# Optimization experiments

Hardware: AMD Instinct MI355X
Metric: run time of the kernel (lower is better)

The kernel has to match this reference:

```python
import jax, jax.numpy as jnp
import numpy as np
import math

B, L, D = 8, 2048, 256


def setup_inputs() -> dict:
    key = jax.random.key(0)
    ks = jax.random.split(key, 8)
    return {
        "query": jax.random.normal(ks[0], (B, L, D), dtype=jnp.float32),
        "key": jax.random.normal(ks[1], (B, L, D), dtype=jnp.float32),
        "value": jax.random.normal(ks[2], (B, L, D), dtype=jnp.float32),
        "mask": jax.random.randint(ks[3], (B, L), 0, 2, dtype=jnp.int32),
        "Wq_w": jax.random.normal(ks[4], (D, D), dtype=jnp.float32) * 0.05,
        "Wq_b": jax.random.normal(ks[5], (D,), dtype=jnp.float32) * 0.05,
        "Wk_w": jax.random.normal(ks[6], (D, D), dtype=jnp.float32) * 0.05,
        "Wk_b": jax.random.normal(ks[7], (D,), dtype=jnp.float32) * 0.05,
    }


def reference(query, key, value, mask, Wq_w, Wq_b, Wk_w, Wk_b):
    d = query.shape[-1]
    q = query @ Wq_w.T + Wq_b            # [B, Lq, D]
    k = key @ Wk_w.T + Wk_b              # [B, Lk, D]
    scores = jnp.einsum("bqd,bkd->bqk", q, k) / math.sqrt(d)  # [B, Lq, Lk]
    m = mask.astype(scores.dtype)[:, None, :]                  # [B, 1, Lk]
    # multiplicative then additive masking, as in original
    scores = jnp.where(m == 0, jnp.asarray(-1e9, scores.dtype), scores * m)
    attn = jax.nn.softmax(scores, axis=-1)
    return jnp.einsum("bqk,bkd->bqd", attn, value)
```

## Files before the change

kernel.cpp:

```cpp
#include <hip/hip_runtime.h>
#include <stdint.h>
#include <stddef.h>

#define B_ 8
#define L_ 2048
#define D_ 256
#define KRANGE 512
#define KTILE 32
#define NITER 16

typedef __bf16 bf16x8 __attribute__((ext_vector_type(8)));
typedef float floatx4 __attribute__((ext_vector_type(4)));
typedef float floatx16 __attribute__((ext_vector_type(16)));
typedef _Float16 half4_t __attribute__((ext_vector_type(4)));
typedef _Float16 half8_t __attribute__((ext_vector_type(8)));

__device__ __forceinline__ short f2bf(float f) {
    union { float f; uint32_t u; } v; v.f = f;
    return (short)((v.u + 0x8000u) >> 16);
}

__device__ __forceinline__ uint32_t pack2bf(float a, float b) {
    union { float f; uint32_t u; } x, y; x.f = a; y.f = b;
    return ((x.u + 0x8000u) >> 16) | ((y.u + 0x8000u) & 0xFFFF0000u);
}

__device__ __forceinline__ uint32_t cvtpk_bf16(float lo, float hi2) {
    uint32_t w;
    asm("v_cvt_pk_bf16_f32 %0, %1, %2" : "=v"(w) : "v"(lo), "v"(hi2));
    return w;
}

__device__ __forceinline__ void pl32swap(uint32_t &a, uint32_t &b) {
    asm("v_permlane32_swap_b32 %0, %1" : "+v"(a), "+v"(b));
}

__device__ __forceinline__ void async16(const void* g, void* l) {
    __builtin_amdgcn_global_load_lds(
        (__attribute__((address_space(1))) void*)g,
        (__attribute__((address_space(3))) void*)l,
        16, 0, 0);
}

__global__ __launch_bounds__(256, 3) void proj_kernel(
    const float* __restrict__ Xq, const float* __restrict__ Xk,
    const float* __restrict__ Wq, const float* __restrict__ Wk,
    const float* __restrict__ bq, const float* __restrict__ bk,
    short* __restrict__ Oq, short* __restrict__ Ok)
{
    const float* X    = blockIdx.y ? Xk : Xq;
    const float* W    = blockIdx.y ? Wk : Wq;
    const float* bias = blockIdx.y ? bk : bq;
    short* Out        = blockIdx.y ? Ok : Oq;

    __shared__ uint32_t As[2][64 * 20];
    __shared__ uint32_t Ws[2][256 * 20];

    const int tid  = threadIdx.x;
    const int wid  = tid >> 6;
    const int lane = tid & 63;
    const int m16  = lane & 15;
    const int quad = lane >> 4;
    const int row0 = blockIdx.x * 64;
    const int ar = tid >> 2, cg = tid & 3;

    floatx4 acc[16];
    const floatx4 z4 = {0.f, 0.f, 0.f, 0.f};
#pragma unroll
    for (int i = 0; i < 16; i++) acc[i] = z4;

    {
        const float* srcA = X + (size_t)(row0 + ar) * D_ + cg * 8;
        float4 a = *(const float4*)srcA, b2 = *(const float4*)(srcA + 4);
        uint4 u; u.x = pack2bf(a.x, a.y); u.y = pack2bf(a.z, a.w);
        u.z = pack2bf(b2.x, b2.y); u.w = pack2bf(b2.z, b2.w);
        *(uint4*)&As[0][ar * 20 + cg * 4] = u;
#pragma unroll
        for (int p = 0; p < 4; p++) {
            const float* srcW = W + (size_t)(p * 64 + ar) * D_ + cg * 8;
            float4 wa = *(const float4*)srcW, wb = *(const float4*)(srcW + 4);
            uint4 w; w.x = pack2bf(wa.x, wa.y); w.y = pack2bf(wa.z, wa.w);
            w.z = pack2bf(wb.x, wb.y); w.w = pack2bf(wb.z, wb.w);
            *(uint4*)&Ws[0][(p * 64 + ar) * 20 + cg * 4] = w;
        }
    }
    __syncthreads();

    for (int kc = 0; kc < 8; kc++) {
        const int buf = kc & 1;
        float4 na, nb, nwa[4], nwb[4];
        if (kc < 7) {
            const int k1 = (kc + 1) * 32;
            const float* srcA = X + (size_t)(row0 + ar) * D_ + k1 + cg * 8;
            na = *(const float4*)srcA; nb = *(const float4*)(srcA + 4);
#pragma unroll
            for (int p = 0; p < 4; p++) {
                const float* srcW = W + (size_t)(p * 64 + ar) * D_ + k1 + cg * 8;
                nwa[p] = *(const float4*)srcW; nwb[p] = *(const float4*)(srcW + 4);
            }
        }
        bf16x8 af = *(const bf16x8*)&As[buf][(wid * 16 + m16) * 20 + quad * 4];
#pragma unroll
        for (int n = 0; n < 16; n++) {
            bf16x8 bfr = *(const bf16x8*)&Ws[buf][(n * 16 + m16) * 20 + quad * 4];
            acc[n] = __builtin_amdgcn_mfma_f32_16x16x32_bf16(af, bfr, acc[n], 0, 0, 0);
        }
        if (kc < 7) {
            uint4 u; u.x = pack2bf(na.x, na.y); u.y = pack2bf(na.z, na.w);
            u.z = pack2bf(nb.x, nb.y); u.w = pack2bf(nb.z, nb.w);
            *(uint4*)&As[buf ^ 1][ar * 20 + cg * 4] = u;
#pragma unroll
            for (int p = 0; p < 4; p++) {
                uint4 w; w.x = pack2bf(nwa[p].x, nwa[p].y); w.y = pack2bf(nwa[p].z, nwa[p].w);
                w.z = pack2bf(nwb[p].x, nwb[p].y); w.w = pack2bf(nwb[p].z, nwb[p].w);
                *(uint4*)&Ws[buf ^ 1][(p * 64 + ar) * 20 + cg * 4] = w;
            }
        }
        __syncthreads();
    }
#pragma unroll
    for (int n = 0; n < 16; n++) {
        const int col = n * 16 + m16;
        const float bv = bias[col];
#pragma unroll
        for (int r = 0; r < 4; r++) {
            const int row = row0 + wid * 16 + quad * 4 + r;
            Out[(size_t)row * D_ + col] = f2bf(acc[n][r] + bv);
        }
    }
}

__global__ __launch_bounds__(256, 2) void vtrans_kernel(
    const float* __restrict__ V, short* __restrict__ Vt)
{
    __shared__ uint32_t T[256 * 20];
    const int tid = threadIdx.x;
    const int b  = blockIdx.y;
    const int l0 = blockIdx.x * 32;
    const int r2 = tid >> 4;
    const int dg = tid & 15;
    const int lp = r2 ^ ((dg & 3) << 2);
#pragma unroll
    for (int p = 0; p < 4; p++) {
        int d0 = (dg + p * 16) * 4;
        const float* src = V + ((size_t)b * L_ + l0 + r2 * 2) * D_ + d0;
        float4 e0 = *(const float4*)src;
        float4 e1 = *(const float4*)(src + D_);
        T[(d0 + 0) * 20 + lp] = pack2bf(e0.x, e1.x);
        T[(d0 + 1) * 20 + lp] = pack2bf(e0.y, e1.y);
        T[(d0 + 2) * 20 + lp] = pack2bf(e0.z, e1.z);
        T[(d0 + 3) * 20 + lp] = pack2bf(e0.w, e1.w);
    }
    __syncthreads();
#pragma unroll
    for (int p = 0; p < 4; p++) {
        int d = (tid >> 2) + p * 64;
        int c = tid & 3;
        int cp = c ^ ((d >> 2) & 3);
        uint4 u = *(const uint4*)&T[d * 20 + cp * 4];
        *(uint4*)(Vt + ((size_t)b * D_ + d) * L_ + l0 + c * 8) = u;
    }
}

__global__ __launch_bounds__(512, 2) void flash_kernel(
    const short* __restrict__ Qb, const short* __restrict__ Kb,
    const short* __restrict__ Vt, const int* __restrict__ mask,
    float* __restrict__ Out, _Float16* __restrict__ Part,
    float* __restrict__ Lpart)
{
    __shared__ short Ks[3][KTILE * 256];
    __shared__ short Vs[3][256 * KTILE];

    const int tid  = threadIdx.x;
    const int wid  = tid >> 6;
    const int lane = tid & 63;
    const int l31  = lane & 31;
    const int hi   = lane >> 5;
    const int b  = blockIdx.x;
    const int yb = blockIdx.y;
    const int q0 = yb * 256;
    const int z  = blockIdx.z;

    const char* kgb = (const char*)(Kb + ((size_t)b * L_ + z * KRANGE) * D_);
    const char* vgb = (const char*)(Vt + (size_t)b * D_ * L_ + z * KRANGE);
    const int*  mg  = mask + b * L_ + z * KRANGE;

    bf16x8 qf[16];
    {
        const short* qrow = Qb + ((size_t)b * L_ + q0 + wid * 32 + l31) * D_ + hi * 8;
#pragma unroll
        for (int dt = 0; dt < 16; dt++)
            qf[dt] = *(const bf16x8*)(qrow + dt * 16);
    }

    uint32_t mbits = 0;
#pragma unroll
    for (int t = 0; t < NITER; t++)
        mbits |= (mg[t * KTILE + l31] != 0 ? 1u : 0u) << t;

    floatx16 o[8];
#pragma unroll
    for (int n = 0; n < 8; n++)
#pragma unroll
        for (int r = 0; r < 16; r++) o[n][r] = 0.f;
    float rsum = 0.f;

    const int KBb = l31 * 512 + ((((l31 & 7) ^ ((l31 >> 3) & 3)) ^ hi) << 4);
    const int VBb = l31 * 64 + (((((l31 >> 1) & 3) ^ ((l31 >> 3) & 1)) ^ hi) << 4);

    int koff[2], voff[2];
#pragma unroll
    for (int c = 0; c < 2; c++) {
        int row = wid * 4 + c * 2 + hi;
        int gk = l31 ^ (row & 7) ^ ((row >> 3) & 3);
        koff[c] = row * 512 + gk * 16;
        int d = (wid * 2 + c) * 16 + (lane >> 2);
        int gv = (lane & 3) ^ ((lane >> 3) & 3) ^ ((lane >> 5) & 1);
        voff[c] = d * (L_ * 2) + gv * 16;
    }

#pragma unroll
    for (int c = 0; c < 2; c++) {
        async16(kgb + koff[c], (char*)&Ks[0][0] + (wid * 2 + c) * 1024);
        async16(vgb + voff[c], (char*)&Vs[2][0] + (wid * 2 + c) * 1024);
        async16(kgb + (KTILE * D_ * 2) + koff[c], (char*)&Ks[1][0] + (wid * 2 + c) * 1024);
        async16(vgb + voff[c], (char*)&Vs[0][0] + (wid * 2 + c) * 1024);
    }
    __builtin_amdgcn_s_waitcnt(0x0F70);
    __syncthreads();

    const float C2 = 0.09016844f;
    bf16x8 pfA, pfB;
    {
        union { uint32_t u[4]; bf16x8 v; } zz;
        zz.u[0] = 0; zz.u[1] = 0; zz.u[2] = 0; zz.u[3] = 0;
        pfA = zz.v; pfB = zz.v;
    }

    short* kCur = &Ks[0][0]; short* kNxt = &Ks[1][0]; short* kDst = &Ks[2][0];
    short* vP   = &Vs[2][0]; short* vQ   = &Vs[0][0]; short* vR   = &Vs[1][0];

    for (int t = 0; t < NITER; t++) {
        {
            const char* kp = kgb + (size_t)((t + 2) & 15) * (KTILE * D_ * 2);
            const char* vp = vgb + (size_t)((t + 1) & 15) * (KTILE * 2);
#pragma unroll
            for (int c = 0; c < 2; c++) {
                async16(kp + koff[c], (char*)kDst + (wid * 2 + c) * 1024);
                async16(vp + voff[c], (char*)vR + (wid * 2 + c) * 1024);
            }
        }

        const char* kl = (const char*)kCur;
        floatx16 s0, s1;
#pragma unroll
        for (int r = 0; r < 16; r++) { s0[r] = 0.f; s1[r] = 0.f; }
        __builtin_amdgcn_s_setprio(1);
#pragma unroll
        for (int dt = 0; dt < 16; dt += 2) {
            bf16x8 kf0 = *(const bf16x8*)(kl + (KBb ^ (dt << 5)));
            bf16x8 kf1 = *(const bf16x8*)(kl + (KBb ^ ((dt + 1) << 5)));
            s0 = __builtin_amdgcn_mfma_f32_32x32x16_bf16(kf0, qf[dt], s0, 0, 0, 0);
            s1 = __builtin_amdgcn_mfma_f32_32x32x16_bf16(kf1, qf[dt + 1], s1, 0, 0, 0);
        }

        const char* vl = (const char*)vP;
#pragma unroll
        for (int n = 0; n < 8; n++) {
            bf16x8 vf0 = *(const bf16x8*)(vl + (VBb ^ (n << 11)));
            bf16x8 vf1 = *(const bf16x8*)(vl + (VBb ^ ((n << 11) | 32)));
            o[n] = __builtin_amdgcn_mfma_f32_32x32x16_bf16(pfA, vf0, o[n], 0, 0, 0);
            o[n] = __builtin_amdgcn_mfma_f32_32x32x16_bf16(pfB, vf1, o[n], 0, 0, 0);
        }
        __builtin_amdgcn_s_setprio(0);

        uint32_t mb = (uint32_t)__ballot((mbits >> t) & 1) >> (hi * 4);
        uint32_t w[8];
#pragma unroll
        for (int i = 0; i < 8; i++) {
            const int r0 = 2 * i, r1 = 2 * i + 1;
            const int k0 = (r0 & 3) + 8 * (r0 >> 2);
            float sv0 = s0[r0] + s1[r0];
            float sv1 = s0[r1] + s1[r1];
            float e0 = ((mb >> k0) & 1) ? exp2f(sv0 * C2) : 0.f;
            float e1 = ((mb >> (k0 + 1)) & 1) ? exp2f(sv1 * C2) : 0.f;
            rsum += e0 + e1;
            w[i] = cvtpk_bf16(e0, e1);
        }
        pl32swap(w[0], w[2]); pl32swap(w[1], w[3]);
        pl32swap(w[4], w[6]); pl32swap(w[5], w[7]);
        {
            union { uint32_t u[4]; bf16x8 v; } ua, ub;
            ua.u[0] = w[0]; ua.u[1] = w[1]; ua.u[2] = w[2]; ua.u[3] = w[3];
            ub.u[0] = w[4]; ub.u[1] = w[5]; ub.u[2] = w[6]; ub.u[3] = w[7];
            pfA = ua.v; pfB = ub.v;
        }

        asm volatile("s_waitcnt vmcnt(4)" ::: "memory");
        __builtin_amdgcn_s_barrier();
        asm volatile("" ::: "memory");

        short* tk = kCur; kCur = kNxt; kNxt = kDst; kDst = tk;
        short* tv = vP;   vP = vQ;     vQ = vR;     vR = tv;
    }

    {
        const char* vl = (const char*)vP;
        __builtin_amdgcn_s_setprio(1);
#pragma unroll
        for (int n = 0; n < 8; n++) {
            bf16x8 vf0 = *(const bf16x8*)(vl + (VBb ^ (n << 11)));
            bf16x8 vf1 = *(const bf16x8*)(vl + (VBb ^ ((n << 11) | 32)));
            o[n] = __builtin_amdgcn_mfma_f32_32x32x16_bf16(pfA, vf0, o[n], 0, 0, 0);
            o[n] = __builtin_amdgcn_mfma_f32_32x32x16_bf16(pfB, vf1, o[n], 0, 0, 0);
        }
        __builtin_amdgcn_s_setprio(0);
    }

    rsum += __shfl_xor(rsum, 32);

    const size_t BLD = (size_t)B_ * L_ * D_;
    const size_t rowbase = (size_t)b * L_ + q0 + wid * 32;
    if (z == 0) {
        float* po = Out + rowbase * D_;
#pragma unroll
        for (int n = 0; n < 8; n++)
#pragma unroll
            for (int r = 0; r < 16; r++) {
                int q = (r & 3) + 8 * (r >> 2) + 4 * hi;
                po[(size_t)q * D_ + n * 32 + l31] = o[n][r];
            }
    } else {
        _Float16* pp = Part + (size_t)(z - 1) * BLD;
#pragma unroll
        for (int n = 0; n < 8; n++)
#pragma unroll
            for (int h2 = 0; h2 < 2; h2++) {
                half8_t hv;
#pragma unroll
                for (int i = 0; i < 8; i++) hv[i] = (_Float16)o[n][h2 * 8 + i];
                size_t cidx = ((((size_t)((b * 8 + yb) * 8 + wid)) * 8 + n) * 2 + h2) * 64 + lane;
                *(half8_t*)(pp + cidx * 8) = hv;
            }
    }
    if (lane < 32) {
        Lpart[(size_t)z * (B_ * L_) + rowbase + lane] = rsum;
    }
}

__global__ __launch_bounds__(256) void norm_kernel(
    float* __restrict__ Out, const _Float16* __restrict__ Part,
    const float* __restrict__ Lpart)
{
    const int gid  = blockIdx.x * 256 + threadIdx.x;
    const int lane = gid & 63;
    const int h2   = (gid >> 6) & 1;
    const int n    = (gid >> 7) & 7;
    const int w    = (gid >> 10) & 7;
    const int yb   = (gid >> 13) & 7;
    const int b    = gid >> 16;
    const int l31  = lane & 31, hi = lane >> 5;
    const int d    = n * 32 + l31;
    const int rowbase = b * L_ + yb * 256 + w * 32;
    const size_t BLD = (size_t)B_ * L_ * D_;
    const int BL = B_ * L_;

    float acc[8];
#pragma unroll
    for (int i = 0; i < 8; i++) acc[i] = 0.f;
#pragma unroll
    for (int zz = 0; zz < 3; zz++) {
        half8_t hv = *(const half8_t*)(Part + zz * BLD + (size_t)gid * 8);
#pragma unroll
        for (int i = 0; i < 8; i++) acc[i] += (float)hv[i];
    }
#pragma unroll
    for (int i = 0; i < 8; i++) {
        const int r = h2 * 8 + i;
        const int q = (r & 3) + 8 * (r >> 2) + 4 * hi;
        const int row = rowbase + q;
        float l = Lpart[row] + Lpart[BL + row] + Lpart[2 * BL + row] + Lpart[3 * BL + row];
        const size_t off = (size_t)row * D_ + d;
        Out[off] = (Out[off] + acc[i]) / l;
    }
}

extern "C" void kernel_launch(void* const* d_in, const int* in_sizes, int n_in,
                              void* d_out, int out_size, void* d_ws, size_t ws_size,
                              hipStream_t stream) {
    const float* query = (const float*)d_in[0];
    const float* key   = (const float*)d_in[1];
    const float* value = (const float*)d_in[2];
    const int*   mask  = (const int*)d_in[3];
    const float* Wq_w  = (const float*)d_in[4];
    const float* Wq_b  = (const float*)d_in[5];
    const float* Wk_w  = (const float*)d_in[6];
    const float* Wk_b  = (const float*)d_in[7];
    float* out = (float*)d_out;

    const size_t BLD = (size_t)B_ * L_ * D_;
    short* qb = (short*)d_ws;
    short* kb = qb + BLD;
    short* vt = kb + BLD;
    _Float16* part = (_Float16*)(vt + BLD);
    float* lpart = (float*)(part + 3 * BLD);

    proj_kernel<<<dim3(256, 2), 256, 0, stream>>>(query, key, Wq_w, Wk_w, Wq_b, Wk_b, qb, kb);
    vtrans_kernel<<<dim3(64, 8), 256, 0, stream>>>(value, vt);
    flash_kernel<<<dim3(8, 8, 4), 512, 0, stream>>>(qb, kb, vt, mask, out, part, lpart);
    norm_kernel<<<dim3((B_ * L_ * D_ / 8) / 256), 256, 0, stream>>>(out, part, lpart);
}
```

Baseline: 167.8 us.

## Fuse projection, V transpose, flash attention and normalization into one cooperative kernel

Replaces four separate kernel launches with a single cooperative kernel of 256 blocks that runs the V transpose, the Q/K projection (retiled to 128 rows per block), flash attention and the split-K normalization as phases separated by grid-wide syncs. The aim is to remove launch overhead and inter-kernel gaps. In exchange it adds the cost of grid.sync, limits the projection and normalization phases to 256 blocks (fewer than before), and raises LDS use to a 96KB static buffer, which may constrain occupancy.

```diff
diff --git a/kernel.cpp b/kernel.cpp
--- a/kernel.cpp
+++ b/kernel.cpp
@@ -1,6 +1,9 @@
 #include <hip/hip_runtime.h>
+#include <hip/hip_cooperative_groups.h>
 #include <stdint.h>
 #include <stddef.h>
+
+namespace cg = cooperative_groups;
 
 #define B_ 8
 #define L_ 2048
@@ -12,7 +15,6 @@
 typedef __bf16 bf16x8 __attribute__((ext_vector_type(8)));
 typedef float floatx4 __attribute__((ext_vector_type(4)));
 typedef float floatx16 __attribute__((ext_vector_type(16)));
-typedef _Float16 half4_t __attribute__((ext_vector_type(4)));
 typedef _Float16 half8_t __attribute__((ext_vector_type(8)));
 
 __device__ __forceinline__ short f2bf(float f) {
@@ -42,346 +44,358 @@
         16, 0, 0);
 }
 
-__global__ __launch_bounds__(256, 3) void proj_kernel(
-    const float* __restrict__ Xq, const float* __restrict__ Xk,
-    const float* __restrict__ Wq, const float* __restrict__ Wk,
-    const float* __restrict__ bq, const float* __restrict__ bk,
-    short* __restrict__ Oq, short* __restrict__ Ok)
+extern "C" __global__ __launch_bounds__(512, 2) void fused_kernel(
+    const float* __restrict__ query, const float* __restrict__ key,
+    const float* __restrict__ value, const int* __restrict__ mask,
+    const float* __restrict__ Wq_w, const float* __restrict__ Wq_b,
+    const float* __restrict__ Wk_w, const float* __restrict__ Wk_b,
+    short* __restrict__ qb, short* __restrict__ kb, short* __restrict__ vt,
+    float* __restrict__ out, _Float16* __restrict__ part,
+    float* __restrict__ lpart)
 {
-    const float* X    = blockIdx.y ? Xk : Xq;
-    const float* W    = blockIdx.y ? Wk : Wq;
-    const float* bias = blockIdx.y ? bk : bq;
-    short* Out        = blockIdx.y ? Ok : Oq;
-
-    __shared__ uint32_t As[2][64 * 20];
-    __shared__ uint32_t Ws[2][256 * 20];
-
-    const int tid  = threadIdx.x;
-    const int wid  = tid >> 6;
-    const int lane = tid & 63;
-    const int m16  = lane & 15;
-    const int quad = lane >> 4;
-    const int row0 = blockIdx.x * 64;
-    const int ar = tid >> 2, cg = tid & 3;
-
-    floatx4 acc[16];
-    const floatx4 z4 = {0.f, 0.f, 0.f, 0.f};
-#pragma unroll
-    for (int i = 0; i < 16; i++) acc[i] = z4;
+    __shared__ char smem[98304];
+
+    cg::grid_group grid = cg::this_grid();
+
+    const int tid = threadIdx.x;
+    const int bid = blockIdx.x + blockIdx.y * 8 + blockIdx.z * 64;
 
     {
-        const float* srcA = X + (size_t)(row0 + ar) * D_ + cg * 8;
-        float4 a = *(const float4*)srcA, b2 = *(const float4*)(srcA + 4);
-        uint4 u; u.x = pack2bf(a.x, a.y); u.y = pack2bf(a.z, a.w);
-        u.z = pack2bf(b2.x, b2.y); u.w = pack2bf(b2.z, b2.w);
-        *(uint4*)&As[0][ar * 20 + cg * 4] = u;
+        uint32_t* T = (uint32_t*)smem + (tid >> 8) * (256 * 20);
+        const int t2 = tid & 255;
+        const int vb = bid * 2 + (tid >> 8);
+        const int b  = vb >> 6;
+        const int l0 = (vb & 63) * 32;
+        const int r2 = t2 >> 4;
+        const int dg = t2 & 15;
+        const int lp = r2 ^ ((dg & 3) << 2);
 #pragma unroll
         for (int p = 0; p < 4; p++) {
-            const float* srcW = W + (size_t)(p * 64 + ar) * D_ + cg * 8;
-            float4 wa = *(const float4*)srcW, wb = *(const float4*)(srcW + 4);
-            uint4 w; w.x = pack2bf(wa.x, wa.y); w.y = pack2bf(wa.z, wa.w);
-            w.z = pack2bf(wb.x, wb.y); w.w = pack2bf(wb.z, wb.w);
-            *(uint4*)&Ws[0][(p * 64 + ar) * 20 + cg * 4] = w;
+            int d0 = (dg + p * 16) * 4;
+            const float* src = value + ((size_t)b * L_ + l0 + r2 * 2) * D_ + d0;
+            float4 e0 = *(const float4*)src;
+            float4 e1 = *(const float4*)(src + D_);
+            T[(d0 + 0) * 20 + lp] = pack2bf(e0.x, e1.x);
+            T[(d0 + 1) * 20 + lp] = pack2bf(e0.y, e1.y);
+            T[(d0 + 2) * 20 + lp] = pack2bf(e0.z, e1.z);
+            T[(d0 + 3) * 20 + lp] = pack2bf(e0.w, e1.w);
+        }
+        __syncthreads();
+#pragma unroll
+        for (int p = 0; p < 4; p++) {
+            int d = (t2 >> 2) + p * 64;
+            int c = t2 & 3;
+            int cp = c ^ ((d >> 2) & 3);
+            uint4 u = *(const uint4*)&T[d * 20 + cp * 4];
+            *(uint4*)(vt + ((size_t)b * D_ + d) * L_ + l0 + c * 8) = u;
         }
     }
     __syncthreads();
 
-    for (int kc = 0; kc < 8; kc++) {
-        const int buf = kc & 1;
-        float4 na, nb, nwa[4], nwb[4];
-        if (kc < 7) {
-            const int k1 = (kc + 1) * 32;
-            const float* srcA = X + (size_t)(row0 + ar) * D_ + k1 + cg * 8;
-            na = *(const float4*)srcA; nb = *(const float4*)(srcA + 4);
-#pragma unroll
-            for (int p = 0; p < 4; p++) {
-                const float* srcW = W + (size_t)(p * 64 + ar) * D_ + k1 + cg * 8;
-                nwa[p] = *(const float4*)srcW; nwb[p] = *(const float4*)(srcW + 4);
-            }
-        }
-        bf16x8 af = *(const bf16x8*)&As[buf][(wid * 16 + m16) * 20 + quad * 4];
+    {
+        const int py = bid >> 7;
+        const int px = bid & 127;
+        const float* X    = py ? key  : query;
+        const float* W    = py ? Wk_w : Wq_w;
+        const float* bias = py ? Wk_b : Wq_b;
+        short* Out        = py ? kb   : qb;
+
+        uint32_t* As = (uint32_t*)smem;
+        uint32_t* Ws = (uint32_t*)smem + 2 * 2560;
+
+        const int wid8 = tid >> 6;
+        const int lane = tid & 63;
+        const int m16  = lane & 15;
+        const int quad = lane >> 4;
+        const int row0 = px * 128;
+        const int ar = tid >> 2, cg2 = tid & 3;
+
+        floatx4 acc[16];
+        const floatx4 z4 = {0.f, 0.f, 0.f, 0.f};
+#pragma unroll
+        for (int i = 0; i < 16; i++) acc[i] = z4;
+
+        {
+            const float* srcA = X + (size_t)(row0 + ar) * D_ + cg2 * 8;
+            float4 a = *(const float4*)srcA, b2 = *(const float4*)(srcA + 4);
+            uint4 u; u.x = pack2bf(a.x, a.y); u.y = pack2bf(a.z, a.w);
+            u.z = pack2bf(b2.x, b2.y); u.w = pack2bf(b2.z, b2.w);
+            *(uint4*)&As[ar * 20 + cg2 * 4] = u;
+#pragma unroll
+            for (int p = 0; p < 2; p++) {
+                const float* srcW = W + (size_t)(p * 128 + ar) * D_ + cg2 * 8;
+                float4 wa = *(const float4*)srcW, wb = *(const float4*)(srcW + 4);
+                uint4 w; w.x = pack2bf(wa.x, wa.y); w.y = pack2bf(wa.z, wa.w);
+                w.z = pack2bf(wb.x, wb.y); w.w = pack2bf(wb.z, wb.w);
+                *(uint4*)&Ws[(p * 128 + ar) * 20 + cg2 * 4] = w;
+            }
+        }
+        __syncthreads();
+
+        for (int kc = 0; kc < 8; kc++) {
+            const int buf = kc & 1;
+            float4 na, nb, nwa[2], nwb[2];
+            if (kc < 7) {
+                const int k1 = (kc + 1) * 32;
+                const float* srcA = X + (size_t)(row0 + ar) * D_ + k1 + cg2 * 8;
+                na = *(const float4*)srcA; nb = *(const float4*)(srcA + 4);
+#pragma unroll
+                for (int p = 0; p < 2; p++) {
+                    const float* srcW = W + (size_t)(p * 128 + ar) * D_ + k1 + cg2 * 8;
+                    nwa[p] = *(const float4*)srcW; nwb[p] = *(const float4*)(srcW + 4);
+                }
+            }
+            bf16x8 af = *(const bf16x8*)&As[buf * 2560 + (wid8 * 16 + m16) * 20 + quad * 4];
+#pragma unroll
+            for (int n = 0; n < 16; n++) {
+                bf16x8 bfr = *(const bf16x8*)&Ws[buf * 5120 + (n * 16 + m16) * 20 + quad * 4];
+                acc[n] = __builtin_amdgcn_mfma_f32_16x16x32_bf16(af, bfr, acc[n], 0, 0, 0);
+            }
+            if (kc < 7) {
+                uint4 u; u.x = pack2bf(na.x, na.y); u.y = pack2bf(na.z, na.w);
+                u.z = pack2bf(nb.x, nb.y); u.w = pack2bf(nb.z, nb.w);
+                *(uint4*)&As[(buf ^ 1) * 2560 + ar * 20 + cg2 * 4] = u;
+#pragma unroll
+                for (int p = 0; p < 2; p++) {
+                    uint4 w; w.x = pack2bf(nwa[p].x, nwa[p].y); w.y = pack2bf(nwa[p].z, nwa[p].w);
+                    w.z = pack2bf(nwb[p].x, nwb[p].y); w.w = pack2bf(nwb[p].z, nwb[p].w);
+                    *(uint4*)&Ws[(buf ^ 1) * 5120 + (p * 128 + ar) * 20 + cg2 * 4] = w;
+                }
+            }
+            __syncthreads();
+        }
 #pragma unroll
         for (int n = 0; n < 16; n++) {
-            bf16x8 bfr = *(const bf16x8*)&Ws[buf][(n * 16 + m16) * 20 + quad * 4];
-            acc[n] = __builtin_amdgcn_mfma_f32_16x16x32_bf16(af, bfr, acc[n], 0, 0, 0);
-        }
-        if (kc < 7) {
-            uint4 u; u.x = pack2bf(na.x, na.y); u.y = pack2bf(na.z, na.w);
-            u.z = pack2bf(nb.x, nb.y); u.w = pack2bf(nb.z, nb.w);
-            *(uint4*)&As[buf ^ 1][ar * 20 + cg * 4] = u;
-#pragma unroll
-            for (int p = 0; p < 4; p++) {
-                uint4 w; w.x = pack2bf(nwa[p].x, nwa[p].y); w.y = pack2bf(nwa[p].z, nwa[p].w);
-                w.z = pack2bf(nwb[p].x, nwb[p].y); w.w = pack2bf(nwb[p].z, nwb[p].w);
-                *(uint4*)&Ws[buf ^ 1][(p * 64 + ar) * 20 + cg * 4] = w;
-            }
-        }
+            const int col = n * 16 + m16;
+            const float bv = bias[col];
+#pragma unroll
+            for (int r = 0; r < 4; r++) {
+                const int row = row0 + wid8 * 16 + quad * 4 + r;
+                Out[(size_t)row * D_ + col] = f2bf(acc[n][r] + bv);
+            }
+        }
+    }
+
+    grid.sync();
+
+    {
+        short* KsB = (short*)smem;
+        short* VsB = KsB + 3 * KTILE * 256;
+
+        const int wid  = tid >> 6;
+        const int lane = tid & 63;
+        const int l31  = lane & 31;
+        const int hi   = lane >> 5;
+        const int b  = blockIdx.x;
+        const int yb = blockIdx.y;
+        const int q0 = yb * 256;
+        const int z  = blockIdx.z;
+
+        const char* kgb = (const char*)(kb + ((size_t)b * L_ + z * KRANGE) * D_);
+        const char* vgb = (const char*)(vt + (size_t)b * D_ * L_ + z * KRANGE);
+        const int*  mg  = mask + b * L_ + z * KRANGE;
+
+        bf16x8 qf[16];
+        {
+            const short* qrow = qb + ((size_t)b * L_ + q0 + wid * 32 + l31) * D_ + hi * 8;
+#pragma unroll
+            for (int dt = 0; dt < 16; dt++)
+                qf[dt] = *(const bf16x8*)(qrow + dt * 16);
+        }
+
+        uint32_t mbits = 0;
+#pragma unroll
+        for (int t = 0; t < NITER; t++)
+            mbits |= (mg[t * KTILE + l31] != 0 ? 1u : 0u) << t;
+
+        floatx16 o[8];
+#pragma unroll
+        for (int n = 0; n < 8; n++)
+#pragma unroll
+            for (int r = 0; r < 16; r++) o[n][r] = 0.f;
+        float rsum = 0.f;
+
+        const int KBb = l31 * 512 + ((((l31 & 7) ^ ((l31 >> 3) & 3)) ^ hi) << 4);
+        const int VBb = l31 * 64 + (((((l31 >> 1) & 3) ^ ((l31 >> 3) & 1)) ^ hi) << 4);
+
+        int koff[2], voff[2];
+#pragma unroll
+        for (int c = 0; c < 2; c++) {
+            int row = wid * 4 + c * 2 + hi;
+            int gk = l31 ^ (row & 7) ^ ((row >> 3) & 3);
+            koff[c] = row * 512 + gk * 16;
+            int d = (wid * 2 + c) * 16 + (lane >> 2);
+            int gv = (lane & 3) ^ ((lane >> 3) & 3) ^ ((lane >> 5) & 1);
+            voff[c] = d * (L_ * 2) + gv * 16;
+        }
+
+#pragma unroll
+        for (int c = 0; c < 2; c++) {
+            async16(kgb + koff[c], (char*)KsB + (wid * 2 + c) * 1024);
+            async16(vgb + voff[c], (char*)(VsB + 2 * 256 * KTILE) + (wid * 2 + c) * 1024);
+            async16(kgb + (KTILE * D_ * 2) + koff[c], (char*)(KsB + KTILE * 256) + (wid * 2 + c) * 1024);
+            async16(vgb + voff[c], (char*)VsB + (wid * 2 + c) * 1024);
+        }
+        __builtin_amdgcn_s_waitcnt(0x0F70);
         __syncthreads();
+
+        const float C2 = 0.09016844f;
+        bf16x8 pfA, pfB;
+        {
+            union { uint32_t u[4]; bf16x8 v; } zz;
+            zz.u[0] = 0; zz.u[1] = 0; zz.u[2] = 0; zz.u[3] = 0;
+            pfA = zz.v; pfB = zz.v;
+        }
+
+        short* kCur = KsB; short* kNxt = KsB + KTILE * 256; short* kDst = KsB + 2 * KTILE * 256;
+        short* vP = VsB + 2 * 256 * KTILE; short* vQ = VsB; short* vR = VsB + 256 * KTILE;
+
+        for (int t = 0; t < NITER; t++) {
+            {
+                const char* kp = kgb + (size_t)((t + 2) & 15) * (KTILE * D_ * 2);
+                const char* vp = vgb + (size_t)((t + 1) & 15) * (KTILE * 2);
+#pragma unroll
+                for (int c = 0; c < 2; c++) {
+                    async16(kp + koff[c], (char*)kDst + (wid * 2 + c) * 1024);
+                    async16(vp + voff[c], (char*)vR + (wid * 2 + c) * 1024);
+                }
+            }
+
+            const char* kl = (const char*)kCur;
+            floatx16 s0, s1;
+#pragma unroll
+            for (int r = 0; r < 16; r++) { s0[r] = 0.f; s1[r] = 0.f; }
+            __builtin_amdgcn_s_setprio(1);
+#pragma unroll
+            for (int dt = 0; dt < 16; dt += 2) {
+                bf16x8 kf0 = *(const bf16x8*)(kl + (KBb ^ (dt << 5)));
+                bf16x8 kf1 = *(const bf16x8*)(kl + (KBb ^ ((dt + 1) << 5)));
+                s0 = __builtin_amdgcn_mfma_f32_32x32x16_bf16(kf0, qf[dt], s0, 0, 0, 0);
+                s1 = __builtin_amdgcn_mfma_f32_32x32x16_bf16(kf1, qf[dt + 1], s1, 0, 0, 0);
+            }
+
+            const char* vl = (const char*)vP;
+#pragma unroll
+            for (int n = 0; n < 8; n++) {
+                bf16x8 vf0 = *(const bf16x8*)(vl + (VBb ^ (n << 11)));
+                bf16x8 vf1 = *(const bf16x8*)(vl + (VBb ^ ((n << 11) | 32)));
+                o[n] = __builtin_amdgcn_mfma_f32_32x32x16_bf16(pfA, vf0, o[n], 0, 0, 0);
+                o[n] = __builtin_amdgcn_mfma_f32_32x32x16_bf16(pfB, vf1, o[n], 0, 0, 0);
+            }
+            __builtin_amdgcn_s_setprio(0);
+
+            uint32_t mb = (uint32_t)__ballot((mbits >> t) & 1) >> (hi * 4);
+            uint32_t w[8];
+#pragma unroll
+            for (int i = 0; i < 8; i++) {
+                const int r0 = 2 * i, r1 = 2 * i + 1;
+                const int k0 = (r0 & 3) + 8 * (r0 >> 2);
+                float sv0 = s0[r0] + s1[r0];
+                float sv1 = s0[r1] + s1[r1];
+                float e0 = ((mb >> k0) & 1) ? exp2f(sv0 * C2) : 0.f;
+                float e1 = ((mb >> (k0 + 1)) & 1) ? exp2f(sv1 * C2) : 0.f;
+                rsum += e0 + e1;
+                w[i] = cvtpk_bf16(e0, e1);
+            }
+            pl32swap(w[0], w[2]); pl32swap(w[1], w[3]);
+            pl32swap(w[4], w[6]); pl32swap(w[5], w[7]);
+            {
+                union { uint32_t u[4]; bf16x8 v; } ua, ub;
+                ua.u[0] = w[0]; ua.u[1] = w[1]; ua.u[2] = w[2]; ua.u[3] = w[3];
+                ub.u[0] = w[4]; ub.u[1] = w[5]; ub.u[2] = w[6]; ub.u[3] = w[7];
+                pfA = ua.v; pfB = ub.v;
+            }
+
+            asm volatile("s_waitcnt vmcnt(4)" ::: "memory");
+            __builtin_amdgcn_s_barrier();
+            asm volatile("" ::: "memory");
+
+            short* tk = kCur; kCur = kNxt; kNxt = kDst; kDst = tk;
+            short* tv = vP;   vP = vQ;     vQ = vR;     vR = tv;
+        }
+
+        {
+            const char* vl = (const char*)vP;
+            __builtin_amdgcn_s_setprio(1);
+#pragma unroll
+            for (int n = 0; n < 8; n++) {
+                bf16x8 vf0 = *(const bf16x8*)(vl + (VBb ^ (n << 11)));
+                bf16x8 vf1 = *(const bf16x8*)(vl + (VBb ^ ((n << 11) | 32)));
+                o[n] = __builtin_amdgcn_mfma_f32_32x32x16_bf16(pfA, vf0, o[n], 0, 0, 0);
+                o[n] = __builtin_amdgcn_mfma_f32_32x32x16_bf16(pfB, vf1, o[n], 0, 0, 0);
+            }
+            __builtin_amdgcn_s_setprio(0);
+        }
+
+        rsum += __shfl_xor(rsum, 32);
+
+        const size_t BLD = (size_t)B_ * L_ * D_;
+        const size_t rowbase = (size_t)b * L_ + q0 + wid * 32;
+        if (z == 0) {
+            float* po = out + rowbase * D_;
+#pragma unroll
+            for (int n = 0; n < 8; n++)
+#pragma unroll
+                for (int r = 0; r < 16; r++) {
+                    int q = (r & 3) + 8 * (r >> 2) + 4 * hi;
+                    po[(size_t)q * D_ + n * 32 + l31] = o[n][r];
+                }
+        } else {
+            _Float16* pp = part + (size_t)(z - 1) * BLD;
+#pragma unroll
+            for (int n = 0; n < 8; n++)
+#pragma unroll
+                for (int h2 = 0; h2 < 2; h2++) {
+                    half8_t hv;
+#pragma unroll
+                    for (int i = 0; i < 8; i++) hv[i] = (_Float16)o[n][h2 * 8 + i];
+                    size_t cidx = ((((size_t)((b * 8 + yb) * 8 + wid)) * 8 + n) * 2 + h2) * 64 + lane;
+                    *(half8_t*)(pp + cidx * 8) = hv;
+                }
+        }
+        if (lane < 32) {
+            lpart[(size_t)z * (B_ * L_) + rowbase + lane] = rsum;
+        }
     }
-#pragma unroll
-    for (int n = 0; n < 16; n++) {
-        const int col = n * 16 + m16;
-        const float bv = bias[col];
-#pragma unroll
-        for (int r = 0; r < 4; r++) {
-            const int row = row0 + wid * 16 + quad * 4 + r;
-            Out[(size_t)row * D_ + col] = f2bf(acc[n][r] + bv);
-        }
-    }
-}
-
-__global__ __launch_bounds__(256, 2) void vtrans_kernel(
-    const float* __restrict__ V, short* __restrict__ Vt)
-{
-    __shared__ uint32_t T[256 * 20];
-    const int tid = threadIdx.x;
-    const int b  = blockIdx.y;
-    const int l0 = blockIdx.x * 32;
-    const int r2 = tid >> 4;
-    const int dg = tid & 15;
-    const int lp = r2 ^ ((dg & 3) << 2);
-#pragma unroll
-    for (int p = 0; p < 4; p++) {
-        int d0 = (dg + p * 16) * 4;
-        const float* src = V + ((size_t)b * L_ + l0 + r2 * 2) * D_ + d0;
-        float4 e0 = *(const float4*)src;
-        float4 e1 = *(const float4*)(src + D_);
-        T[(d0 + 0) * 20 + lp] = pack2bf(e0.x, e1.x);
-        T[(d0 + 1) * 20 + lp] = pack2bf(e0.y, e1.y);
-        T[(d0 + 2) * 20 + lp] = pack2bf(e0.z, e1.z);
-        T[(d0 + 3) * 20 + lp] = pack2bf(e0.w, e1.w);
-    }
-    __syncthreads();
-#pragma unroll
-    for (int p = 0; p < 4; p++) {
-        int d = (tid >> 2) + p * 64;
-        int c = tid & 3;
-        int cp = c ^ ((d >> 2) & 3);
-        uint4 u = *(const uint4*)&T[d * 20 + cp * 4];
-        *(uint4*)(Vt + ((size_t)b * D_ + d) * L_ + l0 + c * 8) = u;
-    }
-}
-
-__global__ __launch_bounds__(512, 2) void flash_kernel(
-    const short* __restrict__ Qb, const short* __restrict__ Kb,
-    const short* __restrict__ Vt, const int* __restrict__ mask,
-    float* __restrict__ Out, _Float16* __restrict__ Part,
-    float* __restrict__ Lpart)
-{
-    __shared__ short Ks[3][KTILE * 256];
-    __shared__ short Vs[3][256 * KTILE];
-
-    const int tid  = threadIdx.x;
-    const int wid  = tid >> 6;
-    const int lane = tid & 63;
-    const int l31  = lane & 31;
-    const int hi   = lane >> 5;
-    const int b  = blockIdx.x;
-    const int yb = blockIdx.y;
-    const int q0 = yb * 256;
-    const int z  = blockIdx.z;
-
-    const char* kgb = (const char*)(Kb + ((size_t)b * L_ + z * KRANGE) * D_);
-    const char* vgb = (const char*)(Vt + (size_t)b * D_ * L_ + z * KRANGE);
-    const int*  mg  = mask + b * L_ + z * KRANGE;
-
-    bf16x8 qf[16];
+
+    grid.sync();
+
     {
-        const short* qrow = Qb + ((size_t)b * L_ + q0 + wid * 32 + l31) * D_ + hi * 8;
-#pragma unroll
-        for (int dt = 0; dt < 16; dt++)
-            qf[dt] = *(const bf16x8*)(qrow + dt * 16);
-    }
-
-    uint32_t mbits = 0;
-#pragma unroll
-    for (int t = 0; t < NITER; t++)
-        mbits |= (mg[t * KTILE + l31] != 0 ? 1u : 0u) << t;
-
-    floatx16 o[8];
-#pragma unroll
-    for (int n = 0; n < 8; n++)
-#pragma unroll
-        for (int r = 0; r < 16; r++) o[n][r] = 0.f;
-    float rsum = 0.f;
-
-    const int KBb = l31 * 512 + ((((l31 & 7) ^ ((l31 >> 3) & 3)) ^ hi) << 4);
-    const int VBb = l31 * 64 + (((((l31 >> 1) & 3) ^ ((l31 >> 3) & 1)) ^ hi) << 4);
-
-    int koff[2], voff[2];
-#pragma unroll
-    for (int c = 0; c < 2; c++) {
-        int row = wid * 4 + c * 2 + hi;
-        int gk = l31 ^ (row & 7) ^ ((row >> 3) & 3);
-        koff[c] = row * 512 + gk * 16;
-        int d = (wid * 2 + c) * 16 + (lane >> 2);
-        int gv = (lane & 3) ^ ((lane >> 3) & 3) ^ ((lane >> 5) & 1);
-        voff[c] = d * (L_ * 2) + gv * 16;
-    }
-
-#pragma unroll
-    for (int c = 0; c < 2; c++) {
-        async16(kgb + koff[c], (char*)&Ks[0][0] + (wid * 2 + c) * 1024);
-        async16(vgb + voff[c], (char*)&Vs[2][0] + (wid * 2 + c) * 1024);
-        async16(kgb + (KTILE * D_ * 2) + koff[c], (char*)&Ks[1][0] + (wid * 2 + c) * 1024);
-        async16(vgb + voff[c], (char*)&Vs[0][0] + (wid * 2 + c) * 1024);
-    }
-    __builtin_amdgcn_s_waitcnt(0x0F70);
-    __syncthreads();
-
-    const float C2 = 0.09016844f;
-    bf16x8 pfA, pfB;
-    {
-        union { uint32_t u[4]; bf16x8 v; } zz;
-        zz.u[0] = 0; zz.u[1] = 0; zz.u[2] = 0; zz.u[3] = 0;
-        pfA = zz.v; pfB = zz.v;
-    }
-
-    short* kCur = &Ks[0][0]; short* kNxt = &Ks[1][0]; short* kDst = &Ks[2][0];
-    short* vP   = &Vs[2][0]; short* vQ   = &Vs[0][0]; short* vR   = &Vs[1][0];
-
-    for (int t = 0; t < NITER; t++) {
-        {
-            const char* kp = kgb + (size_t)((t + 2) & 15) * (KTILE * D_ * 2);
-            const char* vp = vgb + (size_t)((t + 1) & 15) * (KTILE * 2);
-#pragma unroll
-            for (int c = 0; c < 2; c++) {
-                async16(kp + koff[c], (char*)kDst + (wid * 2 + c) * 1024);
-                async16(vp + voff[c], (char*)vR + (wid * 2 + c) * 1024);
-            }
-        }
-
-        const char* kl = (const char*)kCur;
-        floatx16 s0, s1;
-#pragma unroll
-        for (int r = 0; r < 16; r++) { s0[r] = 0.f; s1[r] = 0.f; }
-        __builtin_amdgcn_s_setprio(1);
-#pragma unroll
-        for (int dt = 0; dt < 16; dt += 2) {
-            bf16x8 kf0 = *(const bf16x8*)(kl + (KBb ^ (dt << 5)));
-            bf16x8 kf1 = *(const bf16x8*)(kl + (KBb ^ ((dt + 1) << 5)));
-            s0 = __builtin_amdgcn_mfma_f32_32x32x16_bf16(kf0, qf[dt], s0, 0, 0, 0);
-            s1 = __builtin_amdgcn_mfma_f32_32x32x16_bf16(kf1, qf[dt + 1], s1, 0, 0, 0);
-        }
-
-        const char* vl = (const char*)vP;
-#pragma unroll
-        for (int n = 0; n < 8; n++) {
-            bf16x8 vf0 = *(const bf16x8*)(vl + (VBb ^ (n << 11)));
-            bf16x8 vf1 = *(const bf16x8*)(vl + (VBb ^ ((n << 11) | 32)));
-            o[n] = __builtin_amdgcn_mfma_f32_32x32x16_bf16(pfA, vf0, o[n], 0, 0, 0);
-            o[n] = __builtin_amdgcn_mfma_f32_32x32x16_bf16(pfB, vf1, o[n], 0, 0, 0);
-        }
-        __builtin_amdgcn_s_setprio(0);
-
-        uint32_t mb = (uint32_t)__ballot((mbits >> t) & 1) >> (hi * 4);
-        uint32_t w[8];
-#pragma unroll
-        for (int i = 0; i < 8; i++) {
-            const int r0 = 2 * i, r1 = 2 * i + 1;
-            const int k0 = (r0 & 3) + 8 * (r0 >> 2);
-            float sv0 = s0[r0] + s1[r0];
-            float sv1 = s0[r1] + s1[r1];
-            float e0 = ((mb >> k0) & 1) ? exp2f(sv0 * C2) : 0.f;
-            float e1 = ((mb >> (k0 + 1)) & 1) ? exp2f(sv1 * C2) : 0.f;
-            rsum += e0 + e1;
-            w[i] = cvtpk_bf16(e0, e1);
-        }
-        pl32swap(w[0], w[2]); pl32swap(w[1], w[3]);
-        pl32swap(w[4], w[6]); pl32swap(w[5], w[7]);
-        {
-            union { uint32_t u[4]; bf16x8 v; } ua, ub;
-            ua.u[0] = w[0]; ua.u[1] = w[1]; ua.u[2] = w[2]; ua.u[3] = w[3];
-            ub.u[0] = w[4]; ub.u[1] = w[5]; ub.u[2] = w[6]; ub.u[3] = w[7];
-            pfA = ua.v; pfB = ub.v;
-        }
-
-        asm volatile("s_waitcnt vmcnt(4)" ::: "memory");
-        __builtin_amdgcn_s_barrier();
-        asm volatile("" ::: "memory");
-
-        short* tk = kCur; kCur = kNxt; kNxt = kDst; kDst = tk;
-        short* tv = vP;   vP = vQ;     vQ = vR;     vR = tv;
-    }
-
-    {
-        const char* vl = (const char*)vP;
-        __builtin_amdgcn_s_setprio(1);
-#pragma unroll
-        for (int n = 0; n < 8; n++) {
-            bf16x8 vf0 = *(const bf16x8*)(vl + (VBb ^ (n << 11)));
-            bf16x8 vf1 = *(const bf16x8*)(vl + (VBb ^ ((n << 11) | 32)));
-            o[n] = __builtin_amdgcn_mfma_f32_32x32x16_bf16(pfA, vf0, o[n], 0, 0, 0);
-            o[n] = __builtin_amdgcn_mfma_f32_32x32x16_bf16(pfB, vf1, o[n], 0, 0, 0);
-        }
-        __builtin_amdgcn_s_setprio(0);
-    }
-
-    rsum += __shfl_xor(rsum, 32);
-
-    const size_t BLD = (size_t)B_ * L_ * D_;
-    const size_t rowbase = (size_t)b * L_ + q0 + wid * 32;
-    if (z == 0) {
-        float* po = Out + rowbase * D_;
-#pragma unroll
-        for (int n = 0; n < 8; n++)
-#pragma unroll
-            for (int r = 0; r < 16; r++) {
-                int q = (r & 3) + 8 * (r >> 2) + 4 * hi;
-                po[(size_t)q * D_ + n * 32 + l31] = o[n][r];
-            }
-    } else {
-        _Float16* pp = Part + (size_t)(z - 1) * BLD;
-#pragma unroll
-        for (int n = 0; n < 8; n++)
-#pragma unroll
-            for (int h2 = 0; h2 < 2; h2++) {
-                half8_t hv;
-#pragma unroll
-                for (int i = 0; i < 8; i++) hv[i] = (_Float16)o[n][h2 * 8 + i];
-                size_t cidx = ((((size_t)((b * 8 + yb) * 8 + wid)) * 8 + n) * 2 + h2) * 64 + lane;
-                *(half8_t*)(pp + cidx * 8) = hv;
-            }
-    }
-    if (lane < 32) {
-        Lpart[(size_t)z * (B_ * L_) + rowbase + lane] = rsum;
-    }
-}
-
-__global__ __launch_bounds__(256) void norm_kernel(
-    float* __restrict__ Out, const _Float16* __restrict__ Part,
-    const float* __restrict__ Lpart)
-{
-    const int gid  = blockIdx.x * 256 + threadIdx.x;
-    const int lane = gid & 63;
-    const int h2   = (gid >> 6) & 1;
-    const int n    = (gid >> 7) & 7;
-    const int w    = (gid >> 10) & 7;
-    const int yb   = (gid >> 13) & 7;
-    const int b    = gid >> 16;
-    const int l31  = lane & 31, hi = lane >> 5;
-    const int d    = n * 32 + l31;
-    const int rowbase = b * L_ + yb * 256 + w * 32;
-    const size_t BLD = (size_t)B_ * L_ * D_;
-    const int BL = B_ * L_;
-
-    float acc[8];
-#pragma unroll
-    for (int i = 0; i < 8; i++) acc[i] = 0.f;
-#pragma unroll
-    for (int zz = 0; zz < 3; zz++) {
-        half8_t hv = *(const half8_t*)(Part + zz * BLD + (size_t)gid * 8);
-#pragma unroll
-        for (int i = 0; i < 8; i++) acc[i] += (float)hv[i];
-    }
-#pragma unroll
-    for (int i = 0; i < 8; i++) {
-        const int r = h2 * 8 + i;
-        const int q = (r & 3) + 8 * (r >> 2) + 4 * hi;
-        const int row = rowbase + q;
-        float l = Lpart[row] + Lpart[BL + row] + Lpart[2 * BL + row] + Lpart[3 * BL + row];
-        const size_t off = (size_t)row * D_ + d;
-        Out[off] = (Out[off] + acc[i]) / l;
+        const size_t BLD = (size_t)B_ * L_ * D_;
+        const int BL = B_ * L_;
+        const int base = bid * 512 + tid;
+#pragma unroll
+        for (int k = 0; k < 4; k++) {
+            const int gid  = base + k * 131072;
+            const int lane = gid & 63;
+            const int h2   = (gid >> 6) & 1;
+            const int n    = (gid >> 7) & 7;
+            const int wv   = (gid >> 10) & 7;
+            const int yb   = (gid >> 13) & 7;
+            const int b    = gid >> 16;
+            const int l31  = lane & 31, hi = lane >> 5;
+            const int d    = n * 32 + l31;
+            const int rowbase = b * L_ + yb * 256 + wv * 32;
+
+            float acc[8];
+#pragma unroll
+            for (int i = 0; i < 8; i++) acc[i] = 0.f;
+#pragma unroll
+            for (int zz = 0; zz < 3; zz++) {
+                half8_t hv = *(const half8_t*)(part + zz * BLD + (size_t)gid * 8);
+#pragma unroll
+                for (int i = 0; i < 8; i++) acc[i] += (float)hv[i];
+            }
+#pragma unroll
+            for (int i = 0; i < 8; i++) {
+                const int r = h2 * 8 + i;
+                const int q = (r & 3) + 8 * (r >> 2) + 4 * hi;
+                const int row = rowbase + q;
+                float l = lpart[row] + lpart[BL + row] + lpart[2 * BL + row] + lpart[3 * BL + row];
+                const size_t off = (size_t)row * D_ + d;
+                out[off] = (out[off] + acc[i]) / l;
+            }
+        }
     }
 }
 
@@ -405,8 +419,12 @@
     _Float16* part = (_Float16*)(vt + BLD);
     float* lpart = (float*)(part + 3 * BLD);
 
-    proj_kernel<<<dim3(256, 2), 256, 0, stream>>>(query, key, Wq_w, Wk_w, Wq_b, Wk_b, qb, kb);
-    vtrans_kernel<<<dim3(64, 8), 256, 0, stream>>>(value, vt);
-    flash_kernel<<<dim3(8, 8, 4), 512, 0, stream>>>(qb, kb, vt, mask, out, part, lpart);
-    norm_kernel<<<dim3((B_ * L_ * D_ / 8) / 256), 256, 0, stream>>>(out, part, lpart);
-}
+    void* args[] = {
+        (void*)&query, (void*)&key, (void*)&value, (void*)&mask,
+        (void*)&Wq_w, (void*)&Wq_b, (void*)&Wk_w, (void*)&Wk_b,
+        (void*)&qb, (void*)&kb, (void*)&vt,
+        (void*)&out, (void*)&part, (void*)&lpart
+    };
+    hipLaunchCooperativeKernel((const void*)fused_kernel, dim3(8, 8, 4), dim3(512),
+                               args, 0, stream);
+}
```

Measured after the change: 260.0 us. +54.9%, slower.
